# Kernel optimization log

Hardware: AMD Instinct MI355X
Metric: run time of the kernel (lower is better)

Reference implementation:

```python
import jax, jax.numpy as jnp
import numpy as np
import math

RC = 5.0            # radial cutoff rc_rad
ZETA = [1, 2, 3, 4] # zeta list from configs['zeta']=4

def _angular_consts(z):
    # all (lx,ly,lz) with lx+ly+lz <= z (code generates n in range(z+1) and expands
    # each n into its non-negative integer triples)
    tri = []
    for lx in range(z + 1):
        for ly in range(z + 1 - lx):
            for lz in range(z + 1 - lx - ly):
                tri.append((lx, ly, lz))
    tri = np.array(tri, np.int32)
    n = tri.sum(1)
    # fact_norm = (n!/(lx!ly!lz!)) * (z!/((z-n)! n!)) = z! / ((z-n)! lx! ly! lz!)
    c = np.array([math.factorial(z) / (math.factorial(z - int(s)) * math.factorial(int(a)) * math.factorial(int(b)) * math.factorial(int(d)))
                  for (a, b, d), s in zip(tri, n)], np.float32)
    sign = ((-1.0) ** n).astype(np.float32)  # lambda=-1 channel: (1-cos)^z expansion
    return tri, c, sign

ANG = [_angular_consts(z) for z in ZETA]
silu = jax.nn.silu


def setup_inputs() -> dict:
    key = jax.random.key(0)
    ks = jax.random.split(key, 16)
    nat, npairs, Nrad, nzeta, emb, nelem = 2048, 65536, 8, 4, 4, 4
    feat = (Nrad + Nrad * 2 * nzeta) * emb  # 288
    L = 20.0
    pos = jax.random.uniform(ks[0], (nat, 3), jnp.float32) * L
    cell = L * jnp.eye(3, dtype=jnp.float32)
    i1 = jax.random.randint(ks[1], (npairs,), 0, nat, jnp.int32)
    i2 = jax.random.randint(ks[2], (npairs,), 0, nat, jnp.int32)
    shift = jnp.zeros((npairs, 3), jnp.int32)
    ids = jax.random.randint(ks[3], (nat,), 0, nelem, jnp.int32)
    onehot = jax.nn.one_hot(ids, nelem, dtype=jnp.float32)
    def W(k, i, o):
        return jax.random.normal(k, (i, o), jnp.float32) * 0.1
    return dict(
        positions=pos, cell=cell, species_onehot=onehot,
        sw1=W(ks[4], nelem, 64), sb1=jnp.zeros((64,), jnp.float32),
        sw2=W(ks[5], 64, emb), sb2=jnp.zeros((emb,), jnp.float32),
        rw1=W(ks[6], Nrad, 64), rb1=jnp.zeros((64,), jnp.float32),
        rw2=W(ks[7], 64, (nzeta + 1) * Nrad), rb2=jnp.zeros(((nzeta + 1) * Nrad,), jnp.float32),
        aw1=W(ks[8], feat, 256), ab1=jnp.zeros((256,), jnp.float32),
        aw2=W(ks[9], 256, 128), ab2=jnp.zeros((128,), jnp.float32),
        aw3=W(ks[10], 128, 1), ab3=jnp.zeros((1,), jnp.float32),
        first_atom_idx=i1, second_atom_idx=i2, shift_vectors=shift,
    )


def reference(positions, cell, species_onehot, sw1, sb1, sw2, sb2,
              rw1, rb1, rw2, rb2, aw1, ab1, aw2, ab2, aw3, ab3,
              first_atom_idx, second_atom_idx, shift_vectors):
    nat = positions.shape[0]
    Nrad = rw1.shape[0]
    nzeta = rw2.shape[1] // Nrad - 1
    # pair displacement vectors with PBC shifts
    rij = (positions[second_atom_idx] - positions[first_atom_idx]
           + shift_vectors.astype(jnp.float32) @ cell)            # [P,3]
    r = jnp.sqrt(jnp.sum(rij * rij, axis=-1) + 1e-12)             # [P]
    u = rij / r[:, None]                                          # unit vectors
    fc = jnp.where(r < RC, 0.5 * (jnp.cos(jnp.pi * r / RC) + 1.0), 0.0)
    # Gaussian radial basis -> learned radial functions (silu MLP, linear head)
    centers = jnp.linspace(0.0, RC, Nrad)
    w = RC / Nrad
    basis = jnp.exp(-((r[:, None] - centers) ** 2) / (2.0 * w * w)) * fc[:, None]
    rad = silu(basis @ rw1 + rb1) @ rw2 + rb2
    rad = rad.reshape(-1, nzeta + 1, Nrad) * fc[:, None, None]    # [P, nzeta+1, Nrad]
    # species encoder MLP -> per-atom embedding, gathered onto neighbor side
    semb = silu(species_onehot @ sw1 + sb1) @ sw2 + sb2           # [nat, emb]
    sp = semb[second_atom_idx]                                    # [P, emb]
    seg = lambda v: jax.ops.segment_sum(v, first_atom_idx, num_segments=nat)
    # two-body radial descriptor [nat, Nrad, emb]
    R = seg(rad[:, 0, :, None] * sp[:, None, :])
    feats = [R.reshape(nat, -1)]
    # three-body angular descriptors via multinomial (lx,ly,lz) expansion
    for zi in range(nzeta):
        tri, c, sign = ANG[zi]
        l = jnp.asarray(tri, jnp.float32)                         # [L,3]
        g = jnp.prod(u[:, None, :] ** l[None], axis=-1)           # [P,L] u^lx u^ly u^lz
        t = rad[:, 1 + zi, :, None, None] * g[:, None, :, None] * sp[:, None, None, :]
        G = seg(t)                                                # [nat,Nrad,L,emb]
        G2 = G * G
        Ap = jnp.einsum('inle,l->ine', G2, jnp.asarray(c))        # sum_jk f f (1+cos)^z
        Am = jnp.einsum('inle,l->ine', G2, jnp.asarray(c * sign)) # sum_jk f f (1-cos)^z
        feats += [Ap.reshape(nat, -1), Am.reshape(nat, -1)]
    F = jnp.concatenate(feats, axis=-1)                           # [nat, feature_size]
    h = silu(F @ aw1 + ab1)
    h = silu(h @ aw2 + ab2)
    e = h @ aw3 + ab3                                             # per-atom energies
    return jnp.sum(e)


if __name__ == '__main__':
    out = reference(**setup_inputs())
    print(out)
```

## Files before the change

### kernel.cpp

```cpp
#include <hip/hip_runtime.h>
#include <cmath>

#define NAT  2048
#define NP   65536
#define CAP  64
#define SCAP 8192
#define SSTR 120
#define PPB  256

__constant__ int GLX[70] = {0,
  0,0,0,1,
  0,0,0,0,0,0,1,1,1,2,
  0,0,0,0,0,0,0,0,0,0,1,1,1,1,1,1,2,2,2,3,
  0,0,0,0,0,0,0,0,0,0,0,0,0,0,0,1,1,1,1,1,1,1,1,1,1,2,2,2,2,2,2,3,3,3,4};
__constant__ int GLY[70] = {0,
  0,0,1,0,
  0,0,0,1,1,2,0,0,1,0,
  0,0,0,0,1,1,1,2,2,3,0,0,0,1,1,2,0,0,1,0,
  0,0,0,0,0,1,1,1,1,2,2,2,3,3,4,0,0,0,0,1,1,1,2,2,3,0,0,0,1,1,2,0,0,1,0};
__constant__ int GLZ[70] = {0,
  0,1,0,0,
  0,1,2,0,1,0,0,1,0,0,
  0,1,2,3,0,1,2,0,1,0,0,1,2,0,1,0,0,1,0,0,
  0,1,2,3,4,0,1,2,3,0,1,2,0,1,0,0,1,2,3,0,1,2,0,1,0,0,1,2,0,1,0,0,1,0,0};
__constant__ float C_ALL[69] = {
  1,1,1,1,
  1,2,1,2,2,1,2,2,2,1,
  1,3,3,1,3,6,3,3,3,1,3,6,3,6,6,3,3,3,3,1,
  1,4,6,4,1,4,12,12,4,6,12,6,4,4,1,4,12,12,4,12,24,12,12,12,4,6,12,6,12,12,6,4,4,4,1};
__constant__ float CS_ALL[69] = {
  1,-1,-1,-1,
  1,-2,1,-2,2,1,-2,2,2,1,
  1,-3,3,-1,-3,6,-3,3,-3,-1,-3,6,-3,6,-6,-3,3,-3,-3,-1,
  1,-4,6,-4,1,-4,12,-12,4,6,-12,6,-4,4,1,-4,12,-12,4,12,-24,12,-12,12,4,6,-12,6,-12,12,6,-4,4,4,1};
__constant__ int LTAB[4]    = {4,10,20,35};
__constant__ int CUMTAB[4]  = {0,4,14,34};
__constant__ int BASETAB[4] = {32,160,480,1120};

__device__ __forceinline__ float silu_f(float x){ return x / (1.0f + expf(-x)); }

__global__ void k_zero(int* __restrict__ p){
  const int idx = blockIdx.x*256 + threadIdx.x;
  if (idx < 2050) p[idx] = 0;
}

__global__ __launch_bounds__(256) void k_fstage(
    const float* __restrict__ pos, const float* __restrict__ cell,
    const float* __restrict__ oneh,
    const int* __restrict__ i1, const int* __restrict__ i2,
    const int* __restrict__ sv,
    const float* __restrict__ sw1, const float* __restrict__ sb1,
    const float* __restrict__ sw2, const float* __restrict__ sb2,
    const float* __restrict__ rw1, const float* __restrict__ rb1,
    const float* __restrict__ rw2, const float* __restrict__ rb2,
    int* __restrict__ cursor, int* __restrict__ nflat,
    int* __restrict__ ord_pid, int* __restrict__ ord_flat,
    float* __restrict__ staged)
{
  __shared__ float sembt[4][4];
  __shared__ int   spidL[PPB];
  __shared__ int   nsurvS, baseS;
  __shared__ float geo[8][5];
  __shared__ int   gspec[8];
  __shared__ float basis[8][8];
  __shared__ float hbuf[8][64];

  const int tid = threadIdx.x, lane = tid & 63, wid = tid >> 6;

  {
    float h = silu_f(sb1[lane] + sw1[wid*64 + lane]);
    const float4 w2 = ((const float4*)sw2)[lane];
    float q0=h*w2.x, q1=h*w2.y, q2=h*w2.z, q3=h*w2.w;
#pragma unroll
    for (int off=32; off>0; off>>=1){
      q0 += __shfl_xor(q0, off); q1 += __shfl_xor(q1, off);
      q2 += __shfl_xor(q2, off); q3 += __shfl_xor(q3, off);
    }
    if (lane < 4){
      float v = (lane==0) ? q0+sb2[0] : (lane==1) ? q1+sb2[1]
              : (lane==2) ? q2+sb2[2] : q3+sb2[3];
      sembt[wid][lane] = v;
    }
  }
  if (tid == 0) nsurvS = 0;
  __syncthreads();

  {
    const int p = blockIdx.x*PPB + tid;
    const int a = i1[p], b = i2[p];
    const float s0=(float)sv[p*3+0], s1=(float)sv[p*3+1], s2=(float)sv[p*3+2];
    const float rx = pos[b*3+0]-pos[a*3+0] + s0*cell[0]+s1*cell[3]+s2*cell[6];
    const float ry = pos[b*3+1]-pos[a*3+1] + s0*cell[1]+s1*cell[4]+s2*cell[7];
    const float rz = pos[b*3+2]-pos[a*3+2] + s0*cell[2]+s1*cell[5]+s2*cell[8];
    const float r = sqrtf(rx*rx+ry*ry+rz*rz + 1e-12f);
    if (r < 5.0f){
      int ls = atomicAdd(&nsurvS, 1);
      spidL[ls] = p;
    }
  }
  __syncthreads();
  const int ns = nsurvS;
  if (ns == 0) return;
  if (tid == 0) baseS = atomicAdd(nflat, ns);
  __syncthreads();
  const int fbase = baseS;

  if (tid < ns){
    const int p = spidL[tid];
    const int a = i1[p];
    const int fs = fbase + tid;
    int s = atomicAdd(&cursor[a], 1);
    if (s < CAP){ ord_pid[a*CAP+s] = p; ord_flat[a*CAP+s] = fs; }
  }
  __syncthreads();

  for (int j0=0; j0<ns; j0+=8){
    const int nj = (ns-j0 < 8) ? (ns-j0) : 8;
    if (tid < nj){
      const int p = spidL[j0+tid];
      const int a = i1[p], b = i2[p];
      const float s0=(float)sv[p*3+0], s1=(float)sv[p*3+1], s2=(float)sv[p*3+2];
      const float rx = pos[b*3+0]-pos[a*3+0] + s0*cell[0]+s1*cell[3]+s2*cell[6];
      const float ry = pos[b*3+1]-pos[a*3+1] + s0*cell[1]+s1*cell[4]+s2*cell[7];
      const float rz = pos[b*3+2]-pos[a*3+2] + s0*cell[2]+s1*cell[5]+s2*cell[8];
      const float r  = sqrtf(rx*rx+ry*ry+rz*rz + 1e-12f);
      const float inv= 1.0f/r;
      geo[tid][0]=r; geo[tid][1]=rx*inv; geo[tid][2]=ry*inv; geo[tid][3]=rz*inv;
      geo[tid][4]=0.5f*(cosf(0.6283185307179586f*r)+1.0f);
      const float o1=oneh[b*4+1], o2=oneh[b*4+2], o3=oneh[b*4+3];
      gspec[tid] = (int)(o1 + 2.0f*o2 + 3.0f*o3 + 0.5f);
    }
    __syncthreads();
    if (tid < nj*8){
      const int j=tid>>3, k=tid&7;
      const float d = geo[j][0] - (float)k*(5.0f/7.0f);
      basis[j][k] = expf(-d*d*1.28f)*geo[j][4];
    }
    __syncthreads();
    for (int idx=tid; idx<nj*64; idx+=256){
      const int j=idx>>6, o=idx&63;
      float h = rb1[o];
#pragma unroll
      for (int k=0;k<8;k++) h += basis[j][k]*rw1[k*64+o];
      hbuf[j][o] = silu_f(h);
    }
    __syncthreads();
    const int j0s = j0;
    for (int idx=tid; idx<nj*40; idx+=256){
      const int j=idx/40, n=idx-j*40;
      float racc = rb2[n];
#pragma unroll 8
      for (int o=0;o<64;o++) racc += hbuf[j][o]*rw2[o*40+n];
      const int fs = fbase + j0s + j;
      if (fs < SCAP) staged[(size_t)fs*SSTR + n] = racc*geo[j][4];
    }
    for (int idx=tid; idx<nj*70; idx+=256){
      const int j=idx/70, l=idx-j*70;
      const float ux=geo[j][1], uy=geo[j][2], uz=geo[j][3];
      const int ex=GLX[l], ey=GLY[l], ez=GLZ[l];
      float g=1.f;
      for (int q=0;q<ex;q++) g*=ux;
      for (int q=0;q<ey;q++) g*=uy;
      for (int q=0;q<ez;q++) g*=uz;
      const int fs = fbase + j0s + j;
      if (fs < SCAP) staged[(size_t)fs*SSTR + 40 + l] = g;
    }
    if (tid < nj*4){
      const int j=tid>>2, e=tid&3;
      const int fs = fbase + j0s + j;
      if (fs < SCAP) staged[(size_t)fs*SSTR + 110 + e] = sembt[gspec[j]][e];
    }
    __syncthreads();
  }
}

__global__ __launch_bounds__(256) void k_feat(
    const int* __restrict__ cursor,
    const int* __restrict__ ord_pid, const int* __restrict__ ord_flat,
    const float* __restrict__ staged, float* __restrict__ Fout)
{
  const int atom = blockIdx.x, tid = threadIdx.x;
  __shared__ float G[2240];
  __shared__ float sdata[8][SSTR];
  __shared__ int opid[CAP];
  __shared__ int pslot[CAP];
  __shared__ int sflb[8];

  int cnt = cursor[atom]; if (cnt > CAP) cnt = CAP;
  if (tid < CAP) opid[tid] = (tid < cnt) ? ord_pid[atom*CAP + tid] : 0x7fffffff;
  __syncthreads();
  if (tid < cnt){
    int my = opid[tid]; int rk = 0;
    for (int j=0;j<cnt;j++) rk += (opid[j] < my);
    pslot[rk] = tid;
  }

  float acc[9];
  int ridx[9], gidx[9], eidx[9];
#pragma unroll
  for (int k=0;k<9;k++){
    acc[k]=0.f;
    int a = tid + (k<<8);
    int ri=0, gi=0, ei=0;
    if (a < 32){ ri = a>>2; gi = 0; ei = a&3; }
    else if (a < 2240){
      int b = a-32; int lb, nl, l, n;
      if (b < 128)      { lb=b;      ei=lb&3; nl=lb>>2; l=nl%4;  n=nl/4;  ri=8 +n; gi=1 +l; }
      else if (b < 448) { lb=b-128;  ei=lb&3; nl=lb>>2; l=nl%10; n=nl/10; ri=16+n; gi=5 +l; }
      else if (b < 1088){ lb=b-448;  ei=lb&3; nl=lb>>2; l=nl%20; n=nl/20; ri=24+n; gi=15+l; }
      else              { lb=b-1088; ei=lb&3; nl=lb>>2; l=nl%35; n=nl/35; ri=32+n; gi=35+l; }
    }
    ridx[k]=ri; gidx[k]=gi; eidx[k]=ei;
  }
  __syncthreads();

  for (int c0=0; c0<cnt; c0+=8){
    const int nc = (cnt-c0 < 8) ? (cnt-c0) : 8;
    if (tid < nc) sflb[tid] = ord_flat[atom*CAP + pslot[c0+tid]];
    __syncthreads();
    for (int idx=tid; idx<nc*SSTR; idx+=256){
      int jj = idx/SSTR, i = idx - jj*SSTR;
      int fsl = sflb[jj];
      sdata[jj][i] = (fsl < SCAP) ? staged[(size_t)fsl*SSTR + i] : 0.f;
    }
    __syncthreads();
    for (int jj=0;jj<nc;jj++){
      const float* sd = sdata[jj];
#pragma unroll
      for (int k=0;k<9;k++)
        acc[k] += sd[ridx[k]] * sd[40+gidx[k]] * sd[110+eidx[k]];
    }
    __syncthreads();
  }

#pragma unroll
  for (int k=0;k<9;k++){
    int a = tid + (k<<8);
    if (a < 2240) G[a] = acc[k];
  }
  __syncthreads();

  float* Fo = Fout + atom*288;
  if (tid < 32) Fo[tid] = G[tid];
  if (tid < 128){
    const int zi = tid>>5, n=(tid>>2)&7, e=tid&3;
    const int L = LTAB[zi], cb = CUMTAB[zi], bs = BASETAB[zi];
    float ap=0.f, am=0.f;
    for (int l=0;l<L;l++){
      float v  = G[bs + ((n*L + l)<<2) + e];
      float v2 = v*v;
      ap += C_ALL [cb+l]*v2;
      am += CS_ALL[cb+l]*v2;
    }
    Fo[32 + (zi<<6)      + (n<<2) + e] = ap;
    Fo[32 + (zi<<6) + 32 + (n<<2) + e] = am;
  }
}

__global__ __launch_bounds__(512) void k_mlp2(
    const float* __restrict__ F,
    const float* __restrict__ aw1, const float* __restrict__ ab1,
    const float* __restrict__ aw2, const float* __restrict__ ab2,
    const float* __restrict__ aw3, const float* __restrict__ ab3,
    float* __restrict__ partials, int* __restrict__ done,
    float* __restrict__ out)
{
  const int tid = threadIdx.x;
  const int abase = blockIdx.x*8;
  __shared__ float Fs[8][288];
  __shared__ float P1[2][8][256];
  __shared__ float Hs[8][256];
  __shared__ float P2[4][8][128];
  __shared__ float Ps[8][128];
  __shared__ float es[8];
  __shared__ int winner;

  for (int idx=tid; idx<8*288; idx+=512){
    int a = idx/288, i = idx - a*288;
    Fs[a][i] = F[(abase+a)*288 + i];
  }
  __syncthreads();

  {
    const int o = tid & 255, half = tid >> 8;
    const int i0 = half*144;
    float p1[8];
#pragma unroll
    for (int a=0;a<8;a++) p1[a]=0.f;
    for (int i=i0;i<i0+144;i++){
      float w = aw1[i*256 + o];
#pragma unroll
      for (int a=0;a<8;a++) p1[a] += Fs[a][i]*w;
    }
#pragma unroll
    for (int a=0;a<8;a++) P1[half][a][o] = p1[a];
  }
  __syncthreads();
  {
    const int o = tid & 255, half = tid >> 8;
    if (half == 0){
#pragma unroll
      for (int a=0;a<8;a++)
        Hs[a][o] = silu_f(ab1[o] + P1[0][a][o] + P1[1][a][o]);
    }
  }
  __syncthreads();

  {
    const int o = tid & 127, q = tid >> 7;
    const int i0 = q*64;
    float p2[8];
#pragma unroll
    for (int a=0;a<8;a++) p2[a]=0.f;
    for (int i=i0;i<i0+64;i++){
      float w = aw2[i*128 + o];
#pragma unroll
      for (int a=0;a<8;a++) p2[a] += Hs[a][i]*w;
    }
#pragma unroll
    for (int a=0;a<8;a++) P2[q][a][o] = p2[a];
  }
  __syncthreads();

#pragma unroll
  for (int rep=0; rep<2; rep++){
    int idx = tid + rep*512;
    int a = idx >> 7, o = idx & 127;
    float h2 = ab2[o] + P2[0][a][o] + P2[1][a][o] + P2[2][a][o] + P2[3][a][o];
    Ps[a][o] = silu_f(h2)*aw3[o];
  }
  __syncthreads();

  {
    const int wv = tid >> 6, lane = tid & 63;
    float s = Ps[wv][lane] + Ps[wv][64+lane];
    for (int off=32; off>0; off>>=1) s += __shfl_xor(s, off);
    if (lane == 0) es[wv] = s;
  }
  __syncthreads();
  if (tid == 0){
    float bsum = es[0]+es[1]+es[2]+es[3]+es[4]+es[5]+es[6]+es[7] + 8.0f*ab3[0];
    __hip_atomic_store(&partials[blockIdx.x], bsum,
                       __ATOMIC_RELEASE, __HIP_MEMORY_SCOPE_AGENT);
    int old = __hip_atomic_fetch_add(done, 1, __ATOMIC_ACQ_REL,
                                     __HIP_MEMORY_SCOPE_AGENT);
    winner = (old == (NAT/8) - 1) ? 1 : 0;
  }
  __syncthreads();

  if (winner && tid < 64){
    float s = 0.f;
#pragma unroll
    for (int q=0;q<4;q++)
      s += __hip_atomic_load(&partials[tid*4+q],
                             __ATOMIC_ACQUIRE, __HIP_MEMORY_SCOPE_AGENT);
    for (int off=32; off>0; off>>=1) s += __shfl_xor(s, off);
    if (tid == 0) out[0] = s;
  }
}

extern "C" void kernel_launch(void* const* d_in, const int* in_sizes, int n_in,
                              void* d_out, int out_size, void* d_ws, size_t ws_size,
                              hipStream_t stream) {
  const float* pos  = (const float*)d_in[0];
  const float* cell = (const float*)d_in[1];
  const float* oneh = (const float*)d_in[2];
  const float* sw1  = (const float*)d_in[3];
  const float* sb1  = (const float*)d_in[4];
  const float* sw2  = (const float*)d_in[5];
  const float* sb2  = (const float*)d_in[6];
  const float* rw1  = (const float*)d_in[7];
  const float* rb1  = (const float*)d_in[8];
  const float* rw2  = (const float*)d_in[9];
  const float* rb2  = (const float*)d_in[10];
  const float* aw1  = (const float*)d_in[11];
  const float* ab1  = (const float*)d_in[12];
  const float* aw2  = (const float*)d_in[13];
  const float* ab2  = (const float*)d_in[14];
  const float* aw3  = (const float*)d_in[15];
  const float* ab3  = (const float*)d_in[16];
  const int*   i1   = (const int*)d_in[17];
  const int*   i2   = (const int*)d_in[18];
  const int*   sv   = (const int*)d_in[19];

  char* ws = (char*)d_ws;
  int*   cursor   = (int*)  (ws + 0);
  int*   nflat    = (int*)  (ws + 8192);
  int*   done     = (int*)  (ws + 8196);
  int*   ord_pid  = (int*)  (ws + 8448);
  int*   ord_flat = (int*)  (ws + 532736);
  float* staged   = (float*)(ws + 1057024);
  float* F        = (float*)(ws + 4989184);
  float* partials = (float*)(ws + 7348480);

  k_zero  <<<9,      256, 0, stream>>>(cursor);
  k_fstage<<<NP/PPB, 256, 0, stream>>>(pos, cell, oneh, i1, i2, sv,
                                       sw1, sb1, sw2, sb2,
                                       rw1, rb1, rw2, rb2,
                                       cursor, nflat, ord_pid, ord_flat, staged);
  k_feat  <<<NAT,    256, 0, stream>>>(cursor, ord_pid, ord_flat, staged, F);
  k_mlp2  <<<NAT/8,  512, 0, stream>>>(F, aw1, ab1, aw2, ab2, aw3, ab3,
                                       partials, done, (float*)d_out);
}
```

Baseline: 68.76 us.

## Run per-atom feature kernel as a single 64-thread wavefront without block barriers

The per-atom feature accumulation kernel moves from 256 threads to one 64-lane wavefront per atom. Each lane now holds 35 accumulators, and the index decode is packed into shared-memory codes. The neighbor ordering rank is computed with wavefront shuffles instead of shared arrays. This removes all __syncthreads and the extra shared buffers, trading thread-level parallelism per block for barrier-free execution. It relies on implicit wavefront synchrony for shared-memory reads after writes, and the larger register footprint may reduce occupancy.

```diff
diff --git a/kernel.cpp b/kernel.cpp
--- a/kernel.cpp
+++ b/kernel.cpp
@@ -145,13 +145,12 @@
       hbuf[j][o] = silu_f(h);
     }
     __syncthreads();
-    const int j0s = j0;
     for (int idx=tid; idx<nj*40; idx+=256){
       const int j=idx/40, n=idx-j*40;
       float racc = rb2[n];
 #pragma unroll 8
       for (int o=0;o<64;o++) racc += hbuf[j][o]*rw2[o*40+n];
-      const int fs = fbase + j0s + j;
+      const int fs = fbase + j0 + j;
       if (fs < SCAP) staged[(size_t)fs*SSTR + n] = racc*geo[j][4];
     }
     for (int idx=tid; idx<nj*70; idx+=256){
@@ -162,93 +161,91 @@
       for (int q=0;q<ex;q++) g*=ux;
       for (int q=0;q<ey;q++) g*=uy;
       for (int q=0;q<ez;q++) g*=uz;
-      const int fs = fbase + j0s + j;
+      const int fs = fbase + j0 + j;
       if (fs < SCAP) staged[(size_t)fs*SSTR + 40 + l] = g;
     }
     if (tid < nj*4){
       const int j=tid>>2, e=tid&3;
-      const int fs = fbase + j0s + j;
+      const int fs = fbase + j0 + j;
       if (fs < SCAP) staged[(size_t)fs*SSTR + 110 + e] = sembt[gspec[j]][e];
     }
     __syncthreads();
   }
 }
 
-__global__ __launch_bounds__(256) void k_feat(
+__global__ __launch_bounds__(64) void k_feat64(
     const int* __restrict__ cursor,
     const int* __restrict__ ord_pid, const int* __restrict__ ord_flat,
     const float* __restrict__ staged, float* __restrict__ Fout)
 {
-  const int atom = blockIdx.x, tid = threadIdx.x;
+  const int atom = blockIdx.x, t = threadIdx.x;
   __shared__ float G[2240];
+  __shared__ unsigned int codes[2240];
   __shared__ float sdata[8][SSTR];
-  __shared__ int opid[CAP];
-  __shared__ int pslot[CAP];
-  __shared__ int sflb[8];
-
-  int cnt = cursor[atom]; if (cnt > CAP) cnt = CAP;
-  if (tid < CAP) opid[tid] = (tid < cnt) ? ord_pid[atom*CAP + tid] : 0x7fffffff;
-  __syncthreads();
-  if (tid < cnt){
-    int my = opid[tid]; int rk = 0;
-    for (int j=0;j<cnt;j++) rk += (opid[j] < my);
-    pslot[rk] = tid;
-  }
-
-  float acc[9];
-  int ridx[9], gidx[9], eidx[9];
-#pragma unroll
-  for (int k=0;k<9;k++){
-    acc[k]=0.f;
-    int a = tid + (k<<8);
+  __shared__ int sflat[CAP];
+
+#pragma unroll
+  for (int k=0;k<35;k++){
+    const int s = k*64 + t;
     int ri=0, gi=0, ei=0;
-    if (a < 32){ ri = a>>2; gi = 0; ei = a&3; }
-    else if (a < 2240){
-      int b = a-32; int lb, nl, l, n;
+    if (s < 32){ ri = s>>2; gi = 0; ei = s&3; }
+    else {
+      int b = s-32; int lb, nl, l, n;
       if (b < 128)      { lb=b;      ei=lb&3; nl=lb>>2; l=nl%4;  n=nl/4;  ri=8 +n; gi=1 +l; }
       else if (b < 448) { lb=b-128;  ei=lb&3; nl=lb>>2; l=nl%10; n=nl/10; ri=16+n; gi=5 +l; }
       else if (b < 1088){ lb=b-448;  ei=lb&3; nl=lb>>2; l=nl%20; n=nl/20; ri=24+n; gi=15+l; }
       else              { lb=b-1088; ei=lb&3; nl=lb>>2; l=nl%35; n=nl/35; ri=32+n; gi=35+l; }
     }
-    ridx[k]=ri; gidx[k]=gi; eidx[k]=ei;
-  }
-  __syncthreads();
+    codes[s] = ((unsigned)ri<<9) | ((unsigned)gi<<2) | (unsigned)ei;
+  }
+
+  int cnt = cursor[atom]; if (cnt > CAP) cnt = CAP;
+
+  int mypid = 0x7fffffff, myflat = SCAP;
+  if (t < cnt){ mypid = ord_pid[atom*CAP + t]; myflat = ord_flat[atom*CAP + t]; }
+  int rk = 0;
+  for (int j=0;j<cnt;j++){
+    int pj = __shfl(mypid, j);
+    rk += (pj < mypid) ? 1 : 0;
+  }
+  if (t < cnt) sflat[rk] = myflat;
+
+  float acc[35];
+#pragma unroll
+  for (int k=0;k<35;k++) acc[k] = 0.f;
 
   for (int c0=0; c0<cnt; c0+=8){
     const int nc = (cnt-c0 < 8) ? (cnt-c0) : 8;
-    if (tid < nc) sflb[tid] = ord_flat[atom*CAP + pslot[c0+tid]];
-    __syncthreads();
-    for (int idx=tid; idx<nc*SSTR; idx+=256){
-      int jj = idx/SSTR, i = idx - jj*SSTR;
-      int fsl = sflb[jj];
-      sdata[jj][i] = (fsl < SCAP) ? staged[(size_t)fsl*SSTR + i] : 0.f;
-    }
-    __syncthreads();
-    for (int jj=0;jj<nc;jj++){
-      const float* sd = sdata[jj];
-#pragma unroll
-      for (int k=0;k<9;k++)
-        acc[k] += sd[ridx[k]] * sd[40+gidx[k]] * sd[110+eidx[k]];
-    }
-    __syncthreads();
-  }
-
-#pragma unroll
-  for (int k=0;k<9;k++){
-    int a = tid + (k<<8);
-    if (a < 2240) G[a] = acc[k];
-  }
-  __syncthreads();
+    for (int j=0;j<nc;j++){
+      const int fs = sflat[c0+j];
+      const bool ok = (fs < SCAP);
+      sdata[j][t] = ok ? staged[(size_t)fs*SSTR + t] : 0.f;
+      if (t < SSTR-64) sdata[j][64+t] = ok ? staged[(size_t)fs*SSTR + 64 + t] : 0.f;
+    }
+    for (int j=0;j<nc;j++){
+      const float* sd = sdata[j];
+#pragma unroll
+      for (int k=0;k<35;k++){
+        const unsigned c = codes[k*64 + t];
+        acc[k] += sd[c>>9] * sd[40 + ((c>>2)&127)] * sd[110 + (c&3)];
+      }
+    }
+  }
+
+#pragma unroll
+  for (int k=0;k<35;k++) G[k*64 + t] = acc[k];
 
   float* Fo = Fout + atom*288;
-  if (tid < 32) Fo[tid] = G[tid];
-  if (tid < 128){
-    const int zi = tid>>5, n=(tid>>2)&7, e=tid&3;
+  if (t < 32) Fo[t] = G[t];
+#pragma unroll
+  for (int rep=0; rep<2; rep++){
+    const int o = t + rep*64;
+    const int zi = o>>5, n=(o>>2)&7, e=o&3;
     const int L = LTAB[zi], cb = CUMTAB[zi], bs = BASETAB[zi];
     float ap=0.f, am=0.f;
     for (int l=0;l<L;l++){
-      float v  = G[bs + ((n*L + l)<<2) + e];
-      float v2 = v*v;
+      const float v  = G[bs + ((n*L + l)<<2) + e];
+      const float v2 = v*v;
       ap += C_ALL [cb+l]*v2;
       am += CS_ALL[cb+l]*v2;
     }
@@ -393,12 +390,12 @@
   float* F        = (float*)(ws + 4989184);
   float* partials = (float*)(ws + 7348480);
 
-  k_zero  <<<9,      256, 0, stream>>>(cursor);
-  k_fstage<<<NP/PPB, 256, 0, stream>>>(pos, cell, oneh, i1, i2, sv,
-                                       sw1, sb1, sw2, sb2,
-                                       rw1, rb1, rw2, rb2,
-                                       cursor, nflat, ord_pid, ord_flat, staged);
-  k_feat  <<<NAT,    256, 0, stream>>>(cursor, ord_pid, ord_flat, staged, F);
-  k_mlp2  <<<NAT/8,  512, 0, stream>>>(F, aw1, ab1, aw2, ab2, aw3, ab3,
-                                       partials, done, (float*)d_out);
+  k_zero  <<<9,       256, 0, stream>>>(cursor);
+  k_fstage<<<NP/PPB,  256, 0, stream>>>(pos, cell, oneh, i1, i2, sv,
+                                        sw1, sb1, sw2, sb2,
+                                        rw1, rb1, rw2, rb2,
+                                        cursor, nflat, ord_pid, ord_flat, staged);
+  k_feat64<<<NAT,      64, 0, stream>>>(cursor, ord_pid, ord_flat, staged, F);
+  k_mlp2  <<<NAT/8,   512, 0, stream>>>(F, aw1, ab1, aw2, ab2, aw3, ab3,
+                                        partials, done, (float*)d_out);
 }
```

New measurement: 75.82 us. 10.3% more time.

## Split fused per-8-atom MLP into two shared-memory tiled GEMM kernels

Applied to the files above, without the earlier changes.

Replaces the single MLP kernel, which processed 8 atoms per block and streamed the weights from global memory per block, with two register-tiled GEMM kernels over 32-atom tiles. Each thread computes a 4x4 output block from shared-memory tiles. The hidden layer is written to a global H buffer, and the second kernel folds in silu, the aw3 projection and the final reduction. Loading the weights once per 32 atoms raises weight reuse, but it adds an extra launch, an H round trip through global memory, and fewer blocks (128 and 64) to spread across the device.

```diff
diff --git a/kernel.cpp b/kernel.cpp
--- a/kernel.cpp
+++ b/kernel.cpp
@@ -145,13 +145,12 @@
       hbuf[j][o] = silu_f(h);
     }
     __syncthreads();
-    const int j0s = j0;
     for (int idx=tid; idx<nj*40; idx+=256){
       const int j=idx/40, n=idx-j*40;
       float racc = rb2[n];
 #pragma unroll 8
       for (int o=0;o<64;o++) racc += hbuf[j][o]*rw2[o*40+n];
-      const int fs = fbase + j0s + j;
+      const int fs = fbase + j0 + j;
       if (fs < SCAP) staged[(size_t)fs*SSTR + n] = racc*geo[j][4];
     }
     for (int idx=tid; idx<nj*70; idx+=256){
@@ -162,12 +161,12 @@
       for (int q=0;q<ex;q++) g*=ux;
       for (int q=0;q<ey;q++) g*=uy;
       for (int q=0;q<ez;q++) g*=uz;
-      const int fs = fbase + j0s + j;
+      const int fs = fbase + j0 + j;
       if (fs < SCAP) staged[(size_t)fs*SSTR + 40 + l] = g;
     }
     if (tid < nj*4){
       const int j=tid>>2, e=tid&3;
-      const int fs = fbase + j0s + j;
+      const int fs = fbase + j0 + j;
       if (fs < SCAP) staged[(size_t)fs*SSTR + 110 + e] = sembt[gspec[j]][e];
     }
     __syncthreads();
@@ -257,105 +256,133 @@
   }
 }
 
-__global__ __launch_bounds__(512) void k_mlp2(
-    const float* __restrict__ F,
-    const float* __restrict__ aw1, const float* __restrict__ ab1,
-    const float* __restrict__ aw2, const float* __restrict__ ab2,
-    const float* __restrict__ aw3, const float* __restrict__ ab3,
+__global__ __launch_bounds__(256) void k_gemm1(
+    const float* __restrict__ F, const float* __restrict__ aw1,
+    const float* __restrict__ ab1, float* __restrict__ H)
+{
+  __shared__ float Ft[32][32];
+  __shared__ float Wt[32][128];
+  const int tid = threadIdx.x;
+  const int m0 = (blockIdx.x >> 1)*32, n0 = (blockIdx.x & 1)*128;
+  const int ty = tid >> 5, tx = tid & 31;
+
+  float acc[4][4];
+#pragma unroll
+  for (int i=0;i<4;i++)
+#pragma unroll
+    for (int j=0;j<4;j++) acc[i][j]=0.f;
+
+  for (int k0=0; k0<288; k0+=32){
+    for (int idx=tid; idx<1024; idx+=256){
+      const int r=idx>>5, kk=idx&31;
+      Ft[r][kk] = F[(m0+r)*288 + k0+kk];
+    }
+    for (int idx=tid; idx<4096; idx+=256){
+      const int kk=idx>>7, c=idx&127;
+      Wt[kk][c] = aw1[(k0+kk)*256 + n0+c];
+    }
+    __syncthreads();
+#pragma unroll 8
+    for (int kk=0;kk<32;kk++){
+      const float4 w = *(const float4*)&Wt[kk][tx*4];
+      float fv0=Ft[ty*4+0][kk], fv1=Ft[ty*4+1][kk],
+            fv2=Ft[ty*4+2][kk], fv3=Ft[ty*4+3][kk];
+      acc[0][0]+=fv0*w.x; acc[0][1]+=fv0*w.y; acc[0][2]+=fv0*w.z; acc[0][3]+=fv0*w.w;
+      acc[1][0]+=fv1*w.x; acc[1][1]+=fv1*w.y; acc[1][2]+=fv1*w.z; acc[1][3]+=fv1*w.w;
+      acc[2][0]+=fv2*w.x; acc[2][1]+=fv2*w.y; acc[2][2]+=fv2*w.z; acc[2][3]+=fv2*w.w;
+      acc[3][0]+=fv3*w.x; acc[3][1]+=fv3*w.y; acc[3][2]+=fv3*w.z; acc[3][3]+=fv3*w.w;
+    }
+    __syncthreads();
+  }
+
+  const float4 b = *(const float4*)&ab1[n0 + tx*4];
+#pragma unroll
+  for (int i=0;i<4;i++){
+    float4 o;
+    o.x = silu_f(acc[i][0]+b.x); o.y = silu_f(acc[i][1]+b.y);
+    o.z = silu_f(acc[i][2]+b.z); o.w = silu_f(acc[i][3]+b.w);
+    *(float4*)&H[(m0+ty*4+i)*256 + n0 + tx*4] = o;
+  }
+}
+
+__global__ __launch_bounds__(256) void k_gemm2(
+    const float* __restrict__ H, const float* __restrict__ aw2,
+    const float* __restrict__ ab2, const float* __restrict__ aw3,
+    const float* __restrict__ ab3,
     float* __restrict__ partials, int* __restrict__ done,
     float* __restrict__ out)
 {
+  __shared__ float Ht[32][32];
+  __shared__ float Wt[32][128];
+  __shared__ float rowp[32][32];
+  __shared__ float rsum[32];
+  __shared__ int   winner;
   const int tid = threadIdx.x;
-  const int abase = blockIdx.x*8;
-  __shared__ float Fs[8][288];
-  __shared__ float P1[2][8][256];
-  __shared__ float Hs[8][256];
-  __shared__ float P2[4][8][128];
-  __shared__ float Ps[8][128];
-  __shared__ float es[8];
-  __shared__ int winner;
-
-  for (int idx=tid; idx<8*288; idx+=512){
-    int a = idx/288, i = idx - a*288;
-    Fs[a][i] = F[(abase+a)*288 + i];
-  }
-  __syncthreads();
-
-  {
-    const int o = tid & 255, half = tid >> 8;
-    const int i0 = half*144;
-    float p1[8];
-#pragma unroll
-    for (int a=0;a<8;a++) p1[a]=0.f;
-    for (int i=i0;i<i0+144;i++){
-      float w = aw1[i*256 + o];
-#pragma unroll
-      for (int a=0;a<8;a++) p1[a] += Fs[a][i]*w;
-    }
-#pragma unroll
-    for (int a=0;a<8;a++) P1[half][a][o] = p1[a];
-  }
-  __syncthreads();
-  {
-    const int o = tid & 255, half = tid >> 8;
-    if (half == 0){
-#pragma unroll
-      for (int a=0;a<8;a++)
-        Hs[a][o] = silu_f(ab1[o] + P1[0][a][o] + P1[1][a][o]);
-    }
-  }
-  __syncthreads();
-
-  {
-    const int o = tid & 127, q = tid >> 7;
-    const int i0 = q*64;
-    float p2[8];
-#pragma unroll
-    for (int a=0;a<8;a++) p2[a]=0.f;
-    for (int i=i0;i<i0+64;i++){
-      float w = aw2[i*128 + o];
-#pragma unroll
-      for (int a=0;a<8;a++) p2[a] += Hs[a][i]*w;
-    }
-#pragma unroll
-    for (int a=0;a<8;a++) P2[q][a][o] = p2[a];
-  }
-  __syncthreads();
-
-#pragma unroll
-  for (int rep=0; rep<2; rep++){
-    int idx = tid + rep*512;
-    int a = idx >> 7, o = idx & 127;
-    float h2 = ab2[o] + P2[0][a][o] + P2[1][a][o] + P2[2][a][o] + P2[3][a][o];
-    Ps[a][o] = silu_f(h2)*aw3[o];
-  }
-  __syncthreads();
-
-  {
-    const int wv = tid >> 6, lane = tid & 63;
-    float s = Ps[wv][lane] + Ps[wv][64+lane];
+  const int m0 = blockIdx.x*32;
+  const int ty = tid >> 5, tx = tid & 31;
+
+  float acc[4][4];
+#pragma unroll
+  for (int i=0;i<4;i++)
+#pragma unroll
+    for (int j=0;j<4;j++) acc[i][j]=0.f;
+
+  for (int k0=0; k0<256; k0+=32){
+    for (int idx=tid; idx<1024; idx+=256){
+      const int r=idx>>5, kk=idx&31;
+      Ht[r][kk] = H[(m0+r)*256 + k0+kk];
+    }
+    for (int idx=tid; idx<4096; idx+=256){
+      const int kk=idx>>7, c=idx&127;
+      Wt[kk][c] = aw2[(k0+kk)*128 + c];
+    }
+    __syncthreads();
+#pragma unroll 8
+    for (int kk=0;kk<32;kk++){
+      const float4 w = *(const float4*)&Wt[kk][tx*4];
+      float h0=Ht[ty*4+0][kk], h1=Ht[ty*4+1][kk],
+            h2=Ht[ty*4+2][kk], h3=Ht[ty*4+3][kk];
+      acc[0][0]+=h0*w.x; acc[0][1]+=h0*w.y; acc[0][2]+=h0*w.z; acc[0][3]+=h0*w.w;
+      acc[1][0]+=h1*w.x; acc[1][1]+=h1*w.y; acc[1][2]+=h1*w.z; acc[1][3]+=h1*w.w;
+      acc[2][0]+=h2*w.x; acc[2][1]+=h2*w.y; acc[2][2]+=h2*w.z; acc[2][3]+=h2*w.w;
+      acc[3][0]+=h3*w.x; acc[3][1]+=h3*w.y; acc[3][2]+=h3*w.z; acc[3][3]+=h3*w.w;
+    }
+    __syncthreads();
+  }
+
+  const float4 b  = *(const float4*)&ab2[tx*4];
+  const float4 w3 = *(const float4*)&aw3[tx*4];
+#pragma unroll
+  for (int i=0;i<4;i++){
+    float rp = silu_f(acc[i][0]+b.x)*w3.x + silu_f(acc[i][1]+b.y)*w3.y
+             + silu_f(acc[i][2]+b.z)*w3.z + silu_f(acc[i][3]+b.w)*w3.w;
+    rowp[ty*4+i][tx] = rp;
+  }
+  __syncthreads();
+  if (tid < 32){
+    float s = 0.f;
+#pragma unroll 8
+    for (int t=0;t<32;t++) s += rowp[tid][t];
+    rsum[tid] = s;
+  }
+  __syncthreads();
+  if (tid < 64){
+    float s = (tid < 32) ? rsum[tid] : 0.f;
     for (int off=32; off>0; off>>=1) s += __shfl_xor(s, off);
-    if (lane == 0) es[wv] = s;
-  }
-  __syncthreads();
-  if (tid == 0){
-    float bsum = es[0]+es[1]+es[2]+es[3]+es[4]+es[5]+es[6]+es[7] + 8.0f*ab3[0];
-    __hip_atomic_store(&partials[blockIdx.x], bsum,
-                       __ATOMIC_RELEASE, __HIP_MEMORY_SCOPE_AGENT);
-    int old = __hip_atomic_fetch_add(done, 1, __ATOMIC_ACQ_REL,
-                                     __HIP_MEMORY_SCOPE_AGENT);
-    winner = (old == (NAT/8) - 1) ? 1 : 0;
-  }
-  __syncthreads();
-
+    if (tid == 0){
+      __hip_atomic_store(&partials[blockIdx.x], s,
+                         __ATOMIC_RELEASE, __HIP_MEMORY_SCOPE_AGENT);
+      int old = __hip_atomic_fetch_add(done, 1, __ATOMIC_ACQ_REL,
+                                       __HIP_MEMORY_SCOPE_AGENT);
+      winner = (old == 63) ? 1 : 0;
+    }
+  }
+  __syncthreads();
   if (winner && tid < 64){
-    float s = 0.f;
-#pragma unroll
-    for (int q=0;q<4;q++)
-      s += __hip_atomic_load(&partials[tid*4+q],
-                             __ATOMIC_ACQUIRE, __HIP_MEMORY_SCOPE_AGENT);
+    float s = __hip_atomic_load(&partials[tid],
+                                __ATOMIC_ACQUIRE, __HIP_MEMORY_SCOPE_AGENT);
     for (int off=32; off>0; off>>=1) s += __shfl_xor(s, off);
-    if (tid == 0) out[0] = s;
+    if (tid == 0) out[0] = s + (float)NAT * ab3[0];
   }
 }
 
@@ -391,14 +418,16 @@
   int*   ord_flat = (int*)  (ws + 532736);
   float* staged   = (float*)(ws + 1057024);
   float* F        = (float*)(ws + 4989184);
-  float* partials = (float*)(ws + 7348480);
-
-  k_zero  <<<9,      256, 0, stream>>>(cursor);
-  k_fstage<<<NP/PPB, 256, 0, stream>>>(pos, cell, oneh, i1, i2, sv,
-                                       sw1, sb1, sw2, sb2,
-                                       rw1, rb1, rw2, rb2,
-                                       cursor, nflat, ord_pid, ord_flat, staged);
-  k_feat  <<<NAT,    256, 0, stream>>>(cursor, ord_pid, ord_flat, staged, F);
-  k_mlp2  <<<NAT/8,  512, 0, stream>>>(F, aw1, ab1, aw2, ab2, aw3, ab3,
-                                       partials, done, (float*)d_out);
-}
+  float* H        = (float*)(ws + 7348480);
+  float* partials = (float*)(ws + 9445632);
+
+  k_zero  <<<9,       256, 0, stream>>>(cursor);
+  k_fstage<<<NP/PPB,  256, 0, stream>>>(pos, cell, oneh, i1, i2, sv,
+                                        sw1, sb1, sw2, sb2,
+                                        rw1, rb1, rw2, rb2,
+                                        cursor, nflat, ord_pid, ord_flat, staged);
+  k_feat  <<<NAT,     256, 0, stream>>>(cursor, ord_pid, ord_flat, staged, F);
+  k_gemm1 <<<128,     256, 0, stream>>>(F, aw1, ab1, H);
+  k_gemm2 <<<64,      256, 0, stream>>>(H, aw2, ab2, aw3, ab3,
+                                        partials, done, (float*)d_out);
+}
```

After: 104.4 us. 1.52x slower.
